# Kernel optimization log

Measured on AMD Instinct MI355X. Metric: run time of the kernel, lower is better.

The kernel has to match this reference:

```python
import jax, jax.numpy as jnp
import numpy as np

WF = 0.1
FP = 2
COEF = WF * (1.0 - 0.8) ** FP  # = 0.004


def setup_inputs() -> dict:
    key = jax.random.key(0)
    k1, k2 = jax.random.split(key)
    N = 16777216
    # probabilities in (0,1); shift away from exact 0/1 to keep logs finite
    p = jax.random.uniform(k1, (N,), dtype=jnp.float32, minval=1e-6, maxval=1.0 - 1e-6)
    index = jax.random.randint(k2, (N,), 0, 2, dtype=jnp.int32)
    return {"p": p, "index": index}


def reference(p, index):
    # index==0 -> coef*log(p); index==1 -> coef*log(1-p); else 0
    term = jnp.where(index == 0, jnp.log(p),
                     jnp.where(index == 1, jnp.log1p(-p), jnp.zeros_like(p)))
    coef = jnp.asarray(COEF, dtype=p.dtype)
    return coef * jnp.sum(term)
```

## Files before the change

kernel.cpp:

```cpp
#include <hip/hip_runtime.h>


static constexpr int BLOCK = 256;
static constexpr int GRID  = 4096;
static constexpr float COEF = 0.004f;
static constexpr float LN2  = 0.69314718055994530942f;

typedef float fvec4 __attribute__((ext_vector_type(4)));
typedef int   ivec4 __attribute__((ext_vector_type(4)));

__device__ __forceinline__ float sel_log2(float pv, int iv) {
    return __log2f((iv == 0) ? pv : 1.0f - pv);
}

__global__ __launch_bounds__(BLOCK) void fl_partial(
    const float* __restrict__ p,
    const int*   __restrict__ idx,
    float*       __restrict__ partials,
    int n)
{
    const fvec4* __restrict__ p4 = reinterpret_cast<const fvec4*>(p);
    const ivec4* __restrict__ i4 = reinterpret_cast<const ivec4*>(idx);
    const int n4 = n >> 2;
    const int stride = GRID * BLOCK;
    int i = blockIdx.x * BLOCK + threadIdx.x;

    float acc = 0.0f;
    for (; i < n4; i += stride) {
        fvec4 pv = __builtin_nontemporal_load(&p4[i]);
        ivec4 iv = __builtin_nontemporal_load(&i4[i]);
        acc += sel_log2(pv.x, iv.x);
        acc += sel_log2(pv.y, iv.y);
        acc += sel_log2(pv.z, iv.z);
        acc += sel_log2(pv.w, iv.w);
    }
    if (blockIdx.x == 0 && threadIdx.x == 0) {
        for (int j = n4 << 2; j < n; ++j)
            acc += sel_log2(p[j], idx[j]);
    }

    for (int off = 32; off > 0; off >>= 1)
        acc += __shfl_down(acc, off, 64);

    __shared__ float ws[BLOCK / 64];
    const int lane = threadIdx.x & 63;
    const int wave = threadIdx.x >> 6;
    if (lane == 0) ws[wave] = acc;
    __syncthreads();
    if (threadIdx.x == 0)
        partials[blockIdx.x] = ws[0] + ws[1] + ws[2] + ws[3];
}

__global__ __launch_bounds__(BLOCK) void fl_final(
    const float* __restrict__ partials,
    float*       __restrict__ out)
{
    float acc = 0.0f;
    for (int i = threadIdx.x; i < GRID; i += BLOCK)
        acc += partials[i];
    for (int off = 32; off > 0; off >>= 1)
        acc += __shfl_down(acc, off, 64);

    __shared__ float ws[BLOCK / 64];
    const int lane = threadIdx.x & 63;
    const int wave = threadIdx.x >> 6;
    if (lane == 0) ws[wave] = acc;
    __syncthreads();
    if (threadIdx.x == 0)
        out[0] = (ws[0] + ws[1] + ws[2] + ws[3]) * (COEF * LN2);
}

extern "C" void kernel_launch(void* const* d_in, const int* in_sizes, int n_in,
                              void* d_out, int out_size, void* d_ws, size_t ws_size,
                              hipStream_t stream)
{
    const float* p   = (const float*)d_in[0];
    const int*   idx = (const int*)d_in[1];
    float* partials  = (float*)d_ws;
    const int n = in_sizes[0];

    fl_partial<<<GRID, BLOCK, 0, stream>>>(p, idx, partials, n);
    fl_final<<<1, BLOCK, 0, stream>>>(partials, (float*)d_out);
}
```

Measured before the change: 140.4 us.

## Stream inputs through LDS via global_load_lds with fixed-size fast path

Adds a fast path, taken when n equals GRID*TILE_E*FITERS, that moves each block's tile of p and index into shared memory with direct global-to-LDS 16-byte loads, waits, then reads it back from LDS to compute the log terms. The grid is halved to 2048 blocks, and each block handles four 2048-element tiles. The aim is to cut vector register pressure and load-instruction overhead on a bandwidth-bound stream. The trade-off is a full waitcnt(0) stall per tile with no double-buffering, which removes overlap between loading and compute, and the fast path only matches this exact input size.

```diff
diff --git a/kernel.cpp b/kernel.cpp
--- a/kernel.cpp
+++ b/kernel.cpp
@@ -1,13 +1,18 @@
 #include <hip/hip_runtime.h>
 
 
-static constexpr int BLOCK = 256;
-static constexpr int GRID  = 4096;
+static constexpr int BLOCK  = 256;
+static constexpr int GRID   = 2048;
+static constexpr int TILE_E = 2048;
+static constexpr int FITERS = 4;
 static constexpr float COEF = 0.004f;
 static constexpr float LN2  = 0.69314718055994530942f;
 
 typedef float fvec4 __attribute__((ext_vector_type(4)));
 typedef int   ivec4 __attribute__((ext_vector_type(4)));
+
+typedef const __attribute__((address_space(1))) unsigned int gu32;
+typedef __attribute__((address_space(3))) unsigned int lu32;
 
 __device__ __forceinline__ float sel_log2(float pv, int iv) {
     return __log2f((iv == 0) ? pv : 1.0f - pv);
@@ -19,32 +24,58 @@
     float*       __restrict__ partials,
     int n)
 {
-    const fvec4* __restrict__ p4 = reinterpret_cast<const fvec4*>(p);
-    const ivec4* __restrict__ i4 = reinterpret_cast<const ivec4*>(idx);
-    const int n4 = n >> 2;
-    const int stride = GRID * BLOCK;
-    int i = blockIdx.x * BLOCK + threadIdx.x;
+    __shared__ float pbuf[TILE_E];
+    __shared__ int   ibuf[TILE_E];
+    const int lane = threadIdx.x & 63;
+    const int wave = threadIdx.x >> 6;
 
     float acc = 0.0f;
-    for (; i < n4; i += stride) {
-        fvec4 pv = __builtin_nontemporal_load(&p4[i]);
-        ivec4 iv = __builtin_nontemporal_load(&i4[i]);
-        acc += sel_log2(pv.x, iv.x);
-        acc += sel_log2(pv.y, iv.y);
-        acc += sel_log2(pv.z, iv.z);
-        acc += sel_log2(pv.w, iv.w);
-    }
-    if (blockIdx.x == 0 && threadIdx.x == 0) {
-        for (int j = n4 << 2; j < n; ++j)
-            acc += sel_log2(p[j], idx[j]);
+
+    if (n == GRID * TILE_E * FITERS) {
+        const int woff = wave * 512;
+        for (int t = 0; t < FITERS; ++t) {
+            const long tile_base = ((long)t * GRID + blockIdx.x) * TILE_E;
+#pragma unroll
+            for (int c = 0; c < 2; ++c) {
+                const long e  = tile_base + woff + c * 256 + lane * 4;
+                const int  le = woff + c * 256 + lane * 4;
+                __builtin_amdgcn_global_load_lds((gu32*)(p   + e), (lu32*)(pbuf + le), 16, 0, 0);
+                __builtin_amdgcn_global_load_lds((gu32*)(idx + e), (lu32*)(ibuf + le), 16, 0, 0);
+            }
+            __builtin_amdgcn_s_waitcnt(0);
+#pragma unroll
+            for (int c = 0; c < 2; ++c) {
+                const int le = woff + c * 256 + lane * 4;
+                fvec4 pv = *(const fvec4*)(pbuf + le);
+                ivec4 iv = *(const ivec4*)(ibuf + le);
+                acc += sel_log2(pv.x, iv.x);
+                acc += sel_log2(pv.y, iv.y);
+                acc += sel_log2(pv.z, iv.z);
+                acc += sel_log2(pv.w, iv.w);
+            }
+        }
+    } else {
+        const fvec4* __restrict__ p4 = reinterpret_cast<const fvec4*>(p);
+        const ivec4* __restrict__ i4 = reinterpret_cast<const ivec4*>(idx);
+        const int n4 = n >> 2;
+        const int stride = GRID * BLOCK;
+        for (int i = blockIdx.x * BLOCK + threadIdx.x; i < n4; i += stride) {
+            fvec4 pv = __builtin_nontemporal_load(&p4[i]);
+            ivec4 iv = __builtin_nontemporal_load(&i4[i]);
+            acc += sel_log2(pv.x, iv.x);
+            acc += sel_log2(pv.y, iv.y);
+            acc += sel_log2(pv.z, iv.z);
+            acc += sel_log2(pv.w, iv.w);
+        }
+        if (blockIdx.x == 0 && threadIdx.x == 0)
+            for (int j = n4 << 2; j < n; ++j)
+                acc += sel_log2(p[j], idx[j]);
     }
 
     for (int off = 32; off > 0; off >>= 1)
         acc += __shfl_down(acc, off, 64);
 
     __shared__ float ws[BLOCK / 64];
-    const int lane = threadIdx.x & 63;
-    const int wave = threadIdx.x >> 6;
     if (lane == 0) ws[wave] = acc;
     __syncthreads();
     if (threadIdx.x == 0)
```

After: 145.4 us. 3.6% more time.
